# Optimization experiments

Hardware: AMD Instinct MI355X
Metric: run time of the kernel (lower is better)

The kernel has to match this reference:

```python
import jax, jax.numpy as jnp
import numpy as np

N = 50000    # nodes
E = 800000   # edges (avg degree 16)
D_IN = 32
D = 128      # hidden_dim
L = 3        # num_layers
G = 64       # num graphs (sizes.shape[0])
EPS = 1e-5


def gelu(x):
    return jax.nn.gelu(x, approximate=False)  # torch nn.GELU default = exact erf


def layer_norm(x, g, b):
    mu = jnp.mean(x, axis=-1, keepdims=True)
    var = jnp.mean((x - mu) ** 2, axis=-1, keepdims=True)
    return (x - mu) * jax.lax.rsqrt(var + EPS) * g + b


def setup_inputs() -> dict:
    key = jax.random.key(0)
    ks = jax.random.split(key, 16)
    s = 0.02
    inp = {
        "node_features": jax.random.normal(ks[0], (N, D_IN), jnp.float32),
        "edge_index": jax.random.randint(ks[1], (2, E), 0, N),
        "edge_weight": jax.random.uniform(ks[2], (E,), jnp.float32),
        "batch_index": jnp.sort(jax.random.randint(ks[3], (N,), 0, G)),
        "sizes": jnp.ones((G,), jnp.int32),
        # params
        "W_in": jax.random.normal(ks[4], (D_IN, D), jnp.float32) * s,
        "b_in": jnp.zeros((D,), jnp.float32),
        "edge_W1": jax.random.normal(ks[5], (L, 2 * D + 1, D), jnp.float32) * s,
        "edge_b1": jnp.zeros((L, D), jnp.float32),
        "edge_W2": jax.random.normal(ks[6], (L, D, D), jnp.float32) * s,
        "edge_b2": jnp.zeros((L, D), jnp.float32),
        "upd_W1": jax.random.normal(ks[7], (L, 2 * D, D), jnp.float32) * s,
        "upd_b1": jnp.zeros((L, D), jnp.float32),
        "upd_W2": jax.random.normal(ks[8], (L, D, D), jnp.float32) * s,
        "upd_b2": jnp.zeros((L, D), jnp.float32),
        "gamma": jnp.ones((L, D), jnp.float32),
        "beta": jnp.zeros((L, D), jnp.float32),
    }
    return inp


def reference(node_features, edge_index, edge_weight, batch_index, sizes,
              W_in, b_in, edge_W1, edge_b1, edge_W2, edge_b2,
              upd_W1, upd_b1, upd_W2, upd_b2, gamma, beta):
    num_graphs = sizes.shape[0]
    hidden = gelu(node_features @ W_in + b_in)                      # [N, D]
    src, dst = edge_index[0], edge_index[1]
    ew = edge_weight[:, None]                                        # [E, 1]
    for l in range(L):
        edge_inputs = jnp.concatenate([hidden[src], hidden[dst], ew], axis=1)  # [E, 2D+1]
        messages = gelu(edge_inputs @ edge_W1[l] + edge_b1[l]) @ edge_W2[l] + edge_b2[l]
        aggregated = jax.ops.segment_sum(messages, dst, num_segments=N)        # index_add_
        cat = jnp.concatenate([hidden, aggregated], axis=1)                    # [N, 2D]
        updated = gelu(cat @ upd_W1[l] + upd_b1[l]) @ upd_W2[l] + upd_b2[l]
        hidden = layer_norm(hidden + updated, gamma[l], beta[l])
        # dropout p=0.0 -> identity
    counts = jax.ops.segment_sum(jnp.ones((N,), hidden.dtype), batch_index, num_segments=num_graphs)
    pooled = jax.ops.segment_sum(hidden, batch_index, num_segments=num_graphs)
    pooled = pooled / jnp.clip(counts, 1.0)[:, None]                 # graph mean pool
    return hidden, pooled
```

## Files before the change

kernel.cpp:

```cpp
#include <hip/hip_runtime.h>
#include <math.h>

#define NN 50000
#define NE 800000
#define DIN 32
#define D 128
#define NL 3
#define NG 64
#define LN_EPS 1e-5f
#define SCAN_BLOCKS 196

#define PR_T   48
#define PR_W2P (PR_T + 192)
#define PR_B2P (PR_W2P + 2)
#define PR_WIN (PR_B2P + 16)
#define PR_CNT (PR_WIN + 32)
#define PR_TOTAL (PR_CNT + NE / 256)

#define NBLK_IP 782

typedef unsigned short u16;
typedef __bf16 bf16x8 __attribute__((ext_vector_type(8)));
typedef float f32x4 __attribute__((ext_vector_type(4)));

__device__ __forceinline__ float gelu_f(float x) {
    return 0.5f * x * (1.0f + erff(x * 0.70710678118654752f));
}

__device__ __forceinline__ float gelu_fast(float x) {
    float u = x * x;
    float z = x * fmaf(-0.1029432f, u, -2.3022082f);
    float e = __builtin_amdgcn_exp2f(z);
    float s = __builtin_amdgcn_rcpf(1.0f + e);
    return x * s;
}

__device__ __forceinline__ u16 f2bf(float x) {
    unsigned int u = __float_as_uint(x);
    u += 0x7fffu + ((u >> 16) & 1u);
    return (u16)(u >> 16);
}

__global__ __launch_bounds__(256) void scan_emit_kernel(
    const int* __restrict__ hist, int* __restrict__ row_ptr,
    int* __restrict__ cursor)
{
    __shared__ int sc[256];
    __shared__ int red[256];
    const int t = threadIdx.x;
    const int blk = blockIdx.x;
    const int i = blk * 256 + t;
    int orig = (i < NN) ? hist[i] : 0;
    sc[t] = orig;

    int seg = 0;
    if (t < blk) {
        const int4* hp = (const int4*)(hist + t * 256);
#pragma unroll 8
        for (int m = 0; m < 64; ++m) {
            int4 v = hp[m];
            seg += v.x + v.y + v.z + v.w;
        }
    }
    red[t] = seg;
    __syncthreads();
    for (int off = 128; off > 0; off >>= 1) {
        if (t < off) red[t] += red[t + off];
        __syncthreads();
    }

    for (int off = 1; off < 256; off <<= 1) {
        int v = (t >= off) ? sc[t - off] : 0;
        __syncthreads();
        sc[t] += v;
        __syncthreads();
    }
    if (i < NN) {
        int ex = sc[t] - orig + red[0];
        row_ptr[i] = ex;
        cursor[i] = ex;
    }
    if (i == 0) row_ptr[NN] = NE;
}

__global__ __launch_bounds__(256) void prep_kernel(
    const float* __restrict__ eW1, const float* __restrict__ uW1,
    const float* __restrict__ uW2, const float* __restrict__ eW2,
    const float* __restrict__ eb2, const float* __restrict__ Wi,
    const int* __restrict__ batch, const int* __restrict__ dst,
    u16* __restrict__ PWT, u16* __restrict__ NW1T, u16* __restrict__ uW2T,
    float* __restrict__ nb2p, u16* __restrict__ WinT,
    float* __restrict__ counts, int* __restrict__ hist)
{
    __shared__ __attribute__((aligned(16))) float ldsF[64 * 65];
    const int blk = blockIdx.x;
    const int tid = threadIdx.x;
    if (blk < PR_T) {
        const int region = blk / 12;
        const int rl = blk - region * 12;
        const int l = rl >> 2;
        const int tile = rl & 3;
        const int k0 = (tile >> 1) * 64, n0 = (tile & 1) * 64;
        const float* srcp; u16* dstp; int dstRS;
        if (region == 0)      { srcp = eW1 + (size_t)l * 257 * 128;         dstp = PWT  + (size_t)l * 32768;         dstRS = 128; }
        else if (region == 1) { srcp = eW1 + (size_t)l * 257 * 128 + 16384; dstp = PWT  + (size_t)l * 32768 + 16384; dstRS = 128; }
        else if (region == 2) { srcp = uW1 + (size_t)l * 32768;             dstp = NW1T + (size_t)l * 32768;         dstRS = 256; }
        else                  { srcp = uW2 + (size_t)l * 16384;             dstp = uW2T + (size_t)l * 16384;         dstRS = 128; }
        const int rr = tid >> 6, cc = tid & 63;
#pragma unroll
        for (int it = 0; it < 16; ++it) {
            int row = it * 4 + rr;
            ldsF[row * 65 + cc] = srcp[(size_t)(k0 + row) * 128 + n0 + cc];
        }
        __syncthreads();
#pragma unroll
        for (int it = 0; it < 16; ++it) {
            int row = it * 4 + rr;
            dstp[(size_t)(n0 + row) * dstRS + k0 + cc] = f2bf(ldsF[cc * 65 + row]);
        }
    } else if (blk < PR_W2P) {
        int i = (blk - PR_T) * 256 + tid;
        int l = i / 16384;
        int r = i - l * 16384;
        int k = r >> 7, n = r & 127;
        const float* w2row = eW2 + (size_t)l * 16384 + k * 128;
        const float* u1col = uW1 + (size_t)l * 32768 + 128 * 128 + n;
        float s = 0.f;
#pragma unroll 4
        for (int j = 0; j < 128; ++j) s = fmaf(w2row[j], u1col[j * 128], s);
        NW1T[(size_t)l * 32768 + n * 256 + 128 + k] = f2bf(s);
    } else if (blk < PR_B2P) {
        int i = (blk - PR_W2P) * 256 + tid;
        if (i < NL * 128) {
            int l = i >> 7, n = i & 127;
            const float* b2r = eb2 + l * 128;
            const float* u1col = uW1 + (size_t)l * 32768 + 128 * 128 + n;
            float s = 0.f;
#pragma unroll 4
            for (int j = 0; j < 128; ++j) s = fmaf(b2r[j], u1col[j * 128], s);
            nb2p[l * 128 + n] = s;
        }
    } else if (blk < PR_WIN) {
        int i = (blk - PR_B2P) * 256 + tid;
        int n = i >> 5, k = i & 31;
        WinT[n * 32 + k] = f2bf(Wi[k * 128 + n]);
    } else if (blk < PR_CNT) {
        float* s_counts = ldsF;
        if (tid < NG) s_counts[tid] = 0.f;
        __syncthreads();
        int t = (blk - PR_WIN) * 256 + tid;
        const int chunk = (NN + 8191) / 8192;
        int beg = t * chunk, end = beg + chunk;
        if (end > NN) end = NN;
        if (beg < NN) {
            int cur = batch[beg];
            float cnt = 0.f;
            for (int i2 = beg; i2 < end; ++i2) {
                int b2 = batch[i2];
                if (b2 != cur) { atomicAdd(&s_counts[cur], cnt); cur = b2; cnt = 0.f; }
                cnt += 1.f;
            }
            atomicAdd(&s_counts[cur], cnt);
        }
        __syncthreads();
        if (tid < NG) {
            float v = s_counts[tid];
            if (v != 0.f) atomicAdd(&counts[tid], v);
        }
    } else {
        int e = (blk - PR_CNT) * 256 + tid;
        atomicAdd(&hist[dst[e]], 1);
    }
}

__global__ __launch_bounds__(256) void scatter_inproj_kernel(
    const int* __restrict__ src, const int* __restrict__ dstp,
    const float* __restrict__ ew, int* __restrict__ cursor,
    int2* __restrict__ sEdge,
    const float* __restrict__ X, const u16* __restrict__ WinT,
    const float* __restrict__ b, u16* __restrict__ hbf,
    const u16* __restrict__ PWT, u16* __restrict__ P)
{
    __shared__ __attribute__((aligned(16))) u16 lds[64 * 264];
    const int blk = blockIdx.x;
    const int tid = threadIdx.x;

    if (blk >= NBLK_IP) {
        int e = (blk - NBLK_IP) * 256 + tid;
        int d = dstp[e];
        int pos = atomicAdd(&cursor[d], 1);
        int2 v;
        v.x = src[e] << 9;
        v.y = __float_as_int(ew[e]);
        sEdge[pos] = v;
        return;
    }

    u16* sO  = lds;
    u16* sXb = lds + 64 * 136;
    const int n0 = blk * 64;
    const int e = tid >> 2, q = tid & 3;

    {
        const int n = n0 + e;
        unsigned hiw[4], low[4];
        if (n < NN) {
            const float4* xr = (const float4*)(X + (size_t)n * DIN + q * 8);
            float vv[8];
            *(float4*)(vv) = xr[0];
            *(float4*)(vv + 4) = xr[1];
#pragma unroll
            for (int j = 0; j < 4; ++j) {
                u16 h0 = f2bf(vv[2 * j]), h1 = f2bf(vv[2 * j + 1]);
                float f0 = __uint_as_float((unsigned)h0 << 16);
                float f1 = __uint_as_float((unsigned)h1 << 16);
                u16 l0 = f2bf(vv[2 * j] - f0), l1 = f2bf(vv[2 * j + 1] - f1);
                hiw[j] = (unsigned)h0 | ((unsigned)h1 << 16);
                low[j] = (unsigned)l0 | ((unsigned)l1 << 16);
            }
        } else {
#pragma unroll
            for (int j = 0; j < 4; ++j) { hiw[j] = 0u; low[j] = 0u; }
        }
        *(uint4*)(sXb + e * 72 + q * 8)      = *(uint4*)hiw;
        *(uint4*)(sXb + e * 72 + 32 + q * 8) = *(uint4*)low;
    }
    __syncthreads();

    const int lane = tid & 63;
    const int l15 = lane & 15;
    const int quad = lane >> 4;
    const int w = tid >> 6;

    {
        f32x4 acc1[4][2];
#pragma unroll
        for (int mt = 0; mt < 4; ++mt)
#pragma unroll
            for (int nt = 0; nt < 2; ++nt) acc1[mt][nt] = (f32x4){0.f, 0.f, 0.f, 0.f};

        bf16x8 bfw[2];
#pragma unroll
        for (int nt = 0; nt < 2; ++nt)
            bfw[nt] = *(const bf16x8*)(WinT + (size_t)(w * 32 + nt * 16 + l15) * 32 + quad * 8);
#pragma unroll
        for (int mt = 0; mt < 4; ++mt) {
            bf16x8 ah = *(const bf16x8*)(sXb + (mt * 16 + l15) * 72 + quad * 8);
            bf16x8 al = *(const bf16x8*)(sXb + (mt * 16 + l15) * 72 + 32 + quad * 8);
            acc1[mt][0] = __builtin_amdgcn_mfma_f32_16x16x32_bf16(ah, bfw[0], acc1[mt][0], 0, 0, 0);
            acc1[mt][0] = __builtin_amdgcn_mfma_f32_16x16x32_bf16(al, bfw[0], acc1[mt][0], 0, 0, 0);
            acc1[mt][1] = __builtin_amdgcn_mfma_f32_16x16x32_bf16(ah, bfw[1], acc1[mt][1], 0, 0, 0);
            acc1[mt][1] = __builtin_amdgcn_mfma_f32_16x16x32_bf16(al, bfw[1], acc1[mt][1], 0, 0, 0);
        }
#pragma unroll
        for (int mt = 0; mt < 4; ++mt)
#pragma unroll
            for (int nt = 0; nt < 2; ++nt) {
                const int col = w * 32 + nt * 16 + l15;
                const float bb = b[col];
#pragma unroll
                for (int r = 0; r < 4; ++r) {
                    const int row = mt * 16 + quad * 4 + r;
                    sO[row * 136 + col] = f2bf(gelu_f(acc1[mt][nt][r] + bb));
                }
            }
    }
    __syncthreads();

    {
        const int n = n0 + e;
        if (n < NN) {
            uint4* hp = (uint4*)(hbf + (size_t)n * D);
            const u16* so = sO + e * 136;
#pragma unroll
            for (int c = 0; c < 4; ++c) hp[q + c * 4] = *(const uint4*)(so + (q + c * 4) * 8);
        }
    }

    const int nbase4 = w * 64;

    f32x4 accp[4][4];
#pragma unroll
    for (int mt = 0; mt < 4; ++mt)
#pragma unroll
        for (int nt = 0; nt < 4; ++nt) accp[mt][nt] = (f32x4){0.f, 0.f, 0.f, 0.f};

#pragma unroll
    for (int kb = 0; kb < 128; kb += 32) {
        bf16x8 bf[4];
#pragma unroll
        for (int nt = 0; nt < 4; ++nt)
            bf[nt] = *(const bf16x8*)(PWT + (size_t)(nbase4 + nt * 16 + l15) * 128 + quad * 8 + kb);
#pragma unroll
        for (int mt = 0; mt < 4; ++mt) {
            bf16x8 af = *(const bf16x8*)(sO + (mt * 16 + l15) * 136 + quad * 8 + kb);
#pragma unroll
            for (int nt = 0; nt < 4; ++nt)
                accp[mt][nt] = __builtin_amdgcn_mfma_f32_16x16x32_bf16(af, bf[nt], accp[mt][nt], 0, 0, 0);
        }
    }
    __syncthreads();

    u16* sP = lds;
#pragma unroll
    for (int mt = 0; mt < 4; ++mt)
#pragma unroll
        for (int nt = 0; nt < 4; ++nt) {
            const int col = nbase4 + nt * 16 + l15;
#pragma unroll
            for (int r = 0; r < 4; ++r)
                sP[(mt * 16 + quad * 4 + r) * 264 + col] = f2bf(accp[mt][nt][r]);
        }
    __syncthreads();
    {
        const int n = n0 + e;
        if (n < NN) {
            uint4* op = (uint4*)(P + (size_t)n * 256);
            const u16* sp = sP + e * 264;
#pragma unroll
            for (int c = 0; c < 8; ++c) op[q + c * 4] = *(const uint4*)(sp + (q + c * 4) * 8);
        }
    }
}

__global__ __launch_bounds__(256) void edge_csr_kernel(
    const u16* __restrict__ P, const int2* __restrict__ sEdge,
    const int* __restrict__ row_ptr,
    const float* __restrict__ W1last, const float* __restrict__ b1,
    u16* __restrict__ Sbf)
{
    const int n = (blockIdx.x * 256 + threadIdx.x) >> 6;
    if (n >= NN) return;
    const int lane = threadIdx.x & 63;
    const int c2 = lane * 2;
    const unsigned laneoff = (unsigned)(c2 * 2);
    const char* Pb = (const char*)P;

    const float wl0 = W1last[c2], wl1 = W1last[c2 + 1];
    unsigned p2 = *(const unsigned*)(Pb + ((unsigned)n * 512u + 256u + laneoff));
    const float t20 = __uint_as_float(p2 << 16) + b1[c2];
    const float t21 = __uint_as_float(p2 & 0xffff0000u) + b1[c2 + 1];

    float a0 = 0.f, a1 = 0.f;
    const int beg = row_ptr[n];
    const int m = row_ptr[n + 1] - beg;
    const int2* ep = sEdge + beg;
    int i = 0;
    for (; i + 3 < m; i += 4) {
        int2 q0 = ep[i], q1 = ep[i + 1], q2 = ep[i + 2], q3 = ep[i + 3];
        unsigned pa = *(const unsigned*)(Pb + ((unsigned)q0.x + laneoff));
        unsigned pb = *(const unsigned*)(Pb + ((unsigned)q1.x + laneoff));
        unsigned pc = *(const unsigned*)(Pb + ((unsigned)q2.x + laneoff));
        unsigned pd = *(const unsigned*)(Pb + ((unsigned)q3.x + laneoff));
        float w0 = __int_as_float(q0.y), w1 = __int_as_float(q1.y);
        float w2 = __int_as_float(q2.y), w3 = __int_as_float(q3.y);
        a0 += gelu_fast(fmaf(w0, wl0, __uint_as_float(pa << 16) + t20));
        a1 += gelu_fast(fmaf(w0, wl1, __uint_as_float(pa & 0xffff0000u) + t21));
        a0 += gelu_fast(fmaf(w1, wl0, __uint_as_float(pb << 16) + t20));
        a1 += gelu_fast(fmaf(w1, wl1, __uint_as_float(pb & 0xffff0000u) + t21));
        a0 += gelu_fast(fmaf(w2, wl0, __uint_as_float(pc << 16) + t20));
        a1 += gelu_fast(fmaf(w2, wl1, __uint_as_float(pc & 0xffff0000u) + t21));
        a0 += gelu_fast(fmaf(w3, wl0, __uint_as_float(pd << 16) + t20));
        a1 += gelu_fast(fmaf(w3, wl1, __uint_as_float(pd & 0xffff0000u) + t21));
    }
    for (; i < m; ++i) {
        int2 q0 = ep[i];
        unsigned pa = *(const unsigned*)(Pb + ((unsigned)q0.x + laneoff));
        float w0 = __int_as_float(q0.y);
        a0 += gelu_fast(fmaf(w0, wl0, __uint_as_float(pa << 16) + t20));
        a1 += gelu_fast(fmaf(w0, wl1, __uint_as_float(pa & 0xffff0000u) + t21));
    }
    unsigned pk = (unsigned)f2bf(a0) | ((unsigned)f2bf(a1) << 16);
    *(unsigned*)(Sbf + (size_t)n * D + c2) = pk;
}

__global__ __launch_bounds__(256, 3) void node_mfma_kernel(
    const u16* __restrict__ hbf, const u16* __restrict__ Sbf,
    const int* __restrict__ hist,
    const u16* __restrict__ NW1T, const float* __restrict__ ub1,
    const float* __restrict__ nb2p,
    const u16* __restrict__ W2T, const float* __restrict__ b2,
    const float* __restrict__ gamma, const float* __restrict__ beta,
    float* __restrict__ hidden_out, u16* __restrict__ hbf_out,
    const u16* __restrict__ PWTnext, u16* __restrict__ Pout, int write_f32,
    const int* __restrict__ batch, float* __restrict__ pooled)
{
    __shared__ __attribute__((aligned(16))) u16 ldsA[64 * 136 * 2];
    __shared__ float s_cnt[64];
    __shared__ int s_b[64];
    u16* sHa = ldsA;
    u16* sSb = ldsA + 64 * 136;
    float* sR = (float*)ldsA;
    const int tid = threadIdx.x;
    const int n0 = blockIdx.x * 64;

    if (tid < 64) {
        int n = n0 + tid;
        s_b[tid] = (write_f32 && n < NN) ? batch[n] : -1;
        if (n >= NN) n = NN - 1;
        s_cnt[tid] = (float)hist[n];
    }
    {
        const int e = tid >> 2, q = tid & 3;
        int n = n0 + e; if (n >= NN) n = NN - 1;
        const uint4* hs = (const uint4*)(hbf + (size_t)n * D);
        const uint4* ss = (const uint4*)(Sbf + (size_t)n * D);
#pragma unroll
        for (int j = 0; j < 4; ++j) {
            const int c = q * 4 + j;
            *(uint4*)(sHa + e * 136 + c * 8) = hs[c];
            *(uint4*)(sSb + e * 136 + c * 8) = ss[c];
        }
    }
    __syncthreads();

    const int lane = tid & 63;
    const int l15 = lane & 15;
    const int quad = lane >> 4;
    const int nbase = (tid >> 6) * 32;

    f32x4 acc[4][2];
#pragma unroll
    for (int mt = 0; mt < 4; ++mt)
#pragma unroll
        for (int nt = 0; nt < 2; ++nt) acc[mt][nt] = (f32x4){0.f, 0.f, 0.f, 0.f};

    const u16* bp0 = NW1T + (size_t)(nbase + l15) * 256 + quad * 8;
    const u16* bp1 = bp0 + 16 * 256;
#pragma unroll
    for (int kb = 0; kb < 256; kb += 32) {
        bf16x8 bf0 = *(const bf16x8*)(bp0 + kb);
        bf16x8 bf1 = *(const bf16x8*)(bp1 + kb);
        const u16* abase = (kb < 128) ? sHa : sSb;
        const int kk = kb & 127;
#pragma unroll
        for (int mt = 0; mt < 4; ++mt) {
            bf16x8 af = *(const bf16x8*)(abase + (mt * 16 + l15) * 136 + quad * 8 + kk);
            acc[mt][0] = __builtin_amdgcn_mfma_f32_16x16x32_bf16(af, bf0, acc[mt][0], 0, 0, 0);
            acc[mt][1] = __builtin_amdgcn_mfma_f32_16x16x32_bf16(af, bf1, acc[mt][1], 0, 0, 0);
        }
    }
    __syncthreads();

#pragma unroll
    for (int mt = 0; mt < 4; ++mt)
#pragma unroll
        for (int nt = 0; nt < 2; ++nt) {
            const int col = nbase + nt * 16 + l15;
            const float bb = ub1[col];
            const float bp = nb2p[col];
#pragma unroll
            for (int r = 0; r < 4; ++r) {
                const int row = mt * 16 + quad * 4 + r;
                float v = acc[mt][nt][r] + bb + s_cnt[row] * bp;
                sSb[row * 136 + col] = f2bf(gelu_f(v));
            }
        }
    __syncthreads();

    f32x4 acc2[4][2];
#pragma unroll
    for (int mt = 0; mt < 4; ++mt)
#pragma unroll
        for (int nt = 0; nt < 2; ++nt) acc2[mt][nt] = (f32x4){0.f, 0.f, 0.f, 0.f};

    const u16* cp0 = W2T + (size_t)(nbase + l15) * 128 + quad * 8;
    const u16* cp1 = cp0 + 16 * 128;
#pragma unroll
    for (int kb = 0; kb < 128; kb += 32) {
        bf16x8 bf0 = *(const bf16x8*)(cp0 + kb);
        bf16x8 bf1 = *(const bf16x8*)(cp1 + kb);
#pragma unroll
        for (int mt = 0; mt < 4; ++mt) {
            bf16x8 af = *(const bf16x8*)(sSb + (mt * 16 + l15) * 136 + quad * 8 + kb);
            acc2[mt][0] = __builtin_amdgcn_mfma_f32_16x16x32_bf16(af, bf0, acc2[mt][0], 0, 0, 0);
            acc2[mt][1] = __builtin_amdgcn_mfma_f32_16x16x32_bf16(af, bf1, acc2[mt][1], 0, 0, 0);
        }
    }

#pragma unroll
    for (int mt = 0; mt < 4; ++mt)
#pragma unroll
        for (int nt = 0; nt < 2; ++nt) {
            const int col = nbase + nt * 16 + l15;
            const float bb = b2[col];
#pragma unroll
            for (int r = 0; r < 4; ++r) {
                const int row = mt * 16 + quad * 4 + r;
                float h = __uint_as_float((unsigned)sHa[row * 136 + col] << 16);
                acc2[mt][nt][r] += bb + h;
            }
        }
    __syncthreads();

#pragma unroll
    for (int mt = 0; mt < 4; ++mt)
#pragma unroll
        for (int nt = 0; nt < 2; ++nt) {
            const int col = nbase + nt * 16 + l15;
#pragma unroll
            for (int r = 0; r < 4; ++r)
                sR[(mt * 16 + quad * 4 + r) * 132 + col] = acc2[mt][nt][r];
        }
    __syncthreads();

    {
        const int e = tid >> 2, t4 = tid & 3;
        float* rr = sR + e * 132 + t4 * 32;
        float s1 = 0.f, s2 = 0.f;
        float4 v[8];
#pragma unroll
        for (int i = 0; i < 8; ++i) {
            v[i] = *(const float4*)(rr + i * 4);
            s1 += v[i].x + v[i].y + v[i].z + v[i].w;
            s2 += v[i].x * v[i].x + v[i].y * v[i].y + v[i].z * v[i].z + v[i].w * v[i].w;
        }
        s1 += __shfl_xor(s1, 1); s2 += __shfl_xor(s2, 1);
        s1 += __shfl_xor(s1, 2); s2 += __shfl_xor(s2, 2);
        const float mean = s1 * (1.f / 128.f);
        const float var = s2 * (1.f / 128.f) - mean * mean;
        const float rs = rsqrtf(var + LN_EPS);
        u16* hrow = (u16*)(sR + e * 132);
#pragma unroll
        for (int i = 0; i < 8; ++i) {
            const float4 g = *(const float4*)(gamma + t4 * 32 + i * 4);
            const float4 be = *(const float4*)(beta + t4 * 32 + i * 4);
            float4 o;
            o.x = (v[i].x - mean) * rs * g.x + be.x;
            o.y = (v[i].y - mean) * rs * g.y + be.y;
            o.z = (v[i].z - mean) * rs * g.z + be.z;
            o.w = (v[i].w - mean) * rs * g.w + be.w;
            if (write_f32) {
                *(float4*)(rr + i * 4) = o;
            } else {
                uint2 pk;
                pk.x = (unsigned)f2bf(o.x) | ((unsigned)f2bf(o.y) << 16);
                pk.y = (unsigned)f2bf(o.z) | ((unsigned)f2bf(o.w) << 16);
                *(uint2*)(hrow + t4 * 32 + i * 4) = pk;
            }
        }
    }

    if (write_f32) {
        __syncthreads();
        {
            const int e = tid >> 2, q = tid & 3;
            const int n = n0 + e;
            if (n < NN) {
                float4* op = (float4*)(hidden_out + (size_t)n * D);
                const float* sr = sR + e * 132;
#pragma unroll
                for (int c = 0; c < 8; ++c) op[q + c * 4] = *(const float4*)(sr + (q + c * 4) * 4);
            }
        }
        {
            const int col = tid & 127, half = tid >> 7;
            const int base = half * 32;
            int cur = s_b[base];
            float acc_p = 0.f;
            for (int i = 0; i < 32; ++i) {
                int b = s_b[base + i];
                if (b < 0) break;
                if (b != cur) { atomicAdd(&pooled[cur * D + col], acc_p); cur = b; acc_p = 0.f; }
                acc_p += sR[(base + i) * 132 + col];
            }
            if (cur >= 0) atomicAdd(&pooled[cur * D + col], acc_p);
        }
    } else {
        __syncthreads();
        {
            const int e = tid >> 2, q = tid & 3;
            const int n = n0 + e;
            if (n < NN) {
                uint4* hp = (uint4*)(hbf_out + (size_t)n * D);
                const u16* sh = (const u16*)(sR + e * 132);
#pragma unroll
                for (int c = 0; c < 4; ++c) hp[q + c * 4] = *(const uint4*)(sh + (q + c * 4) * 8);
            }
        }
        if (PWTnext) {
            const int nbase4 = (tid >> 6) * 64;
            const u16* sHn = (const u16*)sR;
            f32x4 accp[4][4];
#pragma unroll
            for (int mt = 0; mt < 4; ++mt)
#pragma unroll
                for (int nt = 0; nt < 4; ++nt) accp[mt][nt] = (f32x4){0.f, 0.f, 0.f, 0.f};

#pragma unroll
            for (int kb = 0; kb < 128; kb += 32) {
                bf16x8 bf[4];
#pragma unroll
                for (int nt = 0; nt < 4; ++nt)
                    bf[nt] = *(const bf16x8*)(PWTnext + (size_t)(nbase4 + nt * 16 + l15) * 128 + quad * 8 + kb);
#pragma unroll
                for (int mt = 0; mt < 4; ++mt) {
                    bf16x8 af = *(const bf16x8*)(sHn + (size_t)(mt * 16 + l15) * 264 + quad * 8 + kb);
#pragma unroll
                    for (int nt = 0; nt < 4; ++nt)
                        accp[mt][nt] = __builtin_amdgcn_mfma_f32_16x16x32_bf16(af, bf[nt], accp[mt][nt], 0, 0, 0);
                }
            }
            __syncthreads();
            u16* sP = ldsA;
#pragma unroll
            for (int mt = 0; mt < 4; ++mt)
#pragma unroll
                for (int nt = 0; nt < 4; ++nt) {
                    const int col = nbase4 + nt * 16 + l15;
#pragma unroll
                    for (int r = 0; r < 4; ++r)
                        sP[(mt * 16 + quad * 4 + r) * 264 + col] = f2bf(accp[mt][nt][r]);
                }
            __syncthreads();
            const int e = tid >> 2, q = tid & 3;
            const int n = n0 + e;
            if (n < NN) {
                uint4* op = (uint4*)(Pout + (size_t)n * 256);
                const u16* sp = sP + e * 264;
#pragma unroll
                for (int c = 0; c < 8; ++c) op[q + c * 4] = *(const uint4*)(sp + (q + c * 4) * 8);
            }
        }
    }
}

__global__ __launch_bounds__(256) void pool_div_kernel(
    float* __restrict__ pooled, const float* __restrict__ counts)
{
    int i = blockIdx.x * 256 + threadIdx.x;
    pooled[i] /= fmaxf(counts[i >> 7], 1.0f);
}

extern "C" void kernel_launch(void* const* d_in, const int* in_sizes, int n_in,
                              void* d_out, int out_size, void* d_ws, size_t ws_size,
                              hipStream_t stream) {
    const float* X     = (const float*)d_in[0];
    const int*   eidx  = (const int*)d_in[1];
    const float* ew    = (const float*)d_in[2];
    const int*   batch = (const int*)d_in[3];
    const float* W_in  = (const float*)d_in[5];
    const float* b_in  = (const float*)d_in[6];
    const float* eW1   = (const float*)d_in[7];
    const float* eb1   = (const float*)d_in[8];
    const float* eW2   = (const float*)d_in[9];
    const float* eb2   = (const float*)d_in[10];
    const float* uW1   = (const float*)d_in[11];
    const float* ub1   = (const float*)d_in[12];
    const float* uW2   = (const float*)d_in[13];
    const float* ub2   = (const float*)d_in[14];
    const float* gamma = (const float*)d_in[15];
    const float* beta  = (const float*)d_in[16];

    float* out_hidden = (float*)d_out;
    float* out_pooled = out_hidden + (size_t)NN * D;

    u16*   hbf  = (u16*)d_ws;
    u16*   P    = hbf + (size_t)NN * D;
    u16*   Sbf  = P + (size_t)NN * 256;
    u16*   PWT  = Sbf + (size_t)NN * D;
    u16*   NW1T = PWT + (size_t)NL * 256 * 128;
    u16*   uW2T = NW1T + (size_t)NL * 128 * 256;
    float* nb2p = (float*)(uW2T + (size_t)NL * 128 * 128);
    u16*   WinT = (u16*)(nb2p + (size_t)NL * 128);
    int*   hist    = (int*)(WinT + 128 * 32);
    int*   row_ptr = hist + NN;
    int*   cursor  = row_ptr + NN + 1;
    int*   bsum    = cursor + NN;
    int*   boff    = bsum + SCAN_BLOCKS;
    int2*  sEdge   = (int2*)(boff + SCAN_BLOCKS + 1);
    float* counts  = (float*)(sEdge + NE);

    const int* src = eidx;
    const int* dst = eidx + NE;

    hipMemsetAsync(hist, 0, (size_t)NN * sizeof(int), stream);
    hipMemsetAsync(out_pooled, 0, (size_t)NG * D * sizeof(float), stream);
    hipMemsetAsync(counts, 0, (size_t)NG * sizeof(float), stream);

    prep_kernel<<<PR_TOTAL, 256, 0, stream>>>(
        eW1, uW1, uW2, eW2, eb2, W_in, batch, dst,
        PWT, NW1T, uW2T, nb2p, WinT, counts, hist);

    scan_emit_kernel<<<SCAN_BLOCKS, 256, 0, stream>>>(hist, row_ptr, cursor);

    scatter_inproj_kernel<<<NBLK_IP + NE / 256, 256, 0, stream>>>(
        src, dst, ew, cursor, sEdge, X, WinT, b_in, hbf, PWT, P);

    const int nblk = (NN + 63) / 64;
    for (int l = 0; l < NL; ++l) {
        edge_csr_kernel<<<(NN * 64 + 255) / 256, 256, 0, stream>>>(
            P, sEdge, row_ptr,
            eW1 + (size_t)l * 257 * 128 + 256 * 128,
            eb1 + (size_t)l * D, Sbf);
        const u16* pwt_next = (l < NL - 1) ? (PWT + (size_t)(l + 1) * 256 * 128) : nullptr;
        node_mfma_kernel<<<nblk, 256, 0, stream>>>(
            hbf, Sbf, hist,
            NW1T + (size_t)l * 128 * 256, ub1 + (size_t)l * D, nb2p + (size_t)l * D,
            uW2T + (size_t)l * 128 * 128, ub2 + (size_t)l * D,
            gamma + (size_t)l * D, beta + (size_t)l * D,
            out_hidden, hbf, pwt_next, P, (l == NL - 1) ? 1 : 0,
            batch, out_pooled);
    }

    pool_div_kernel<<<(NG * D) / 256, 256, 0, stream>>>(out_pooled, counts);
}
```

Baseline: 457.1 us.

## Split next-layer projection GEMM into two halves to cut accumulator registers

The projection of the new hidden state onto the next layer's edge weights is computed in two passes of 128 output columns each, with 4x2 accumulator tiles instead of 4x4. The first half is staged into the unused upper part of the LDS row while the hidden tile is still being read, and the second half overwrites the lower part after a barrier. Launch bounds are raised from 3 to 4 blocks per SIMD, so the compiler must fit fewer registers and occupancy can rise. This trades repeated A-operand LDS reads and a less register-blocked MFMA loop for lower register pressure, with possible spilling elsewhere in the kernel.

```diff
diff --git a/kernel.cpp b/kernel.cpp
--- a/kernel.cpp
+++ b/kernel.cpp
@@ -374,7 +374,7 @@
     *(unsigned*)(Sbf + (size_t)n * D + c2) = pk;
 }
 
-__global__ __launch_bounds__(256, 3) void node_mfma_kernel(
+__global__ __launch_bounds__(256, 4) void node_mfma_kernel(
     const u16* __restrict__ hbf, const u16* __restrict__ Sbf,
     const int* __restrict__ hist,
     const u16* __restrict__ NW1T, const float* __restrict__ ub1,
@@ -579,47 +579,73 @@
             }
         }
         if (PWTnext) {
-            const int nbase4 = (tid >> 6) * 64;
             const u16* sHn = (const u16*)sR;
-            f32x4 accp[4][4];
+            u16* sPx = (u16*)sR;
+            const int cbase = (tid >> 6) * 32;
+            f32x4 accp[4][2];
+
 #pragma unroll
             for (int mt = 0; mt < 4; ++mt)
 #pragma unroll
-                for (int nt = 0; nt < 4; ++nt) accp[mt][nt] = (f32x4){0.f, 0.f, 0.f, 0.f};
-
+                for (int nt = 0; nt < 2; ++nt) accp[mt][nt] = (f32x4){0.f, 0.f, 0.f, 0.f};
 #pragma unroll
             for (int kb = 0; kb < 128; kb += 32) {
-                bf16x8 bf[4];
-#pragma unroll
-                for (int nt = 0; nt < 4; ++nt)
-                    bf[nt] = *(const bf16x8*)(PWTnext + (size_t)(nbase4 + nt * 16 + l15) * 128 + quad * 8 + kb);
+                bf16x8 bf0 = *(const bf16x8*)(PWTnext + (size_t)(cbase + l15) * 128 + quad * 8 + kb);
+                bf16x8 bf1 = *(const bf16x8*)(PWTnext + (size_t)(cbase + 16 + l15) * 128 + quad * 8 + kb);
 #pragma unroll
                 for (int mt = 0; mt < 4; ++mt) {
                     bf16x8 af = *(const bf16x8*)(sHn + (size_t)(mt * 16 + l15) * 264 + quad * 8 + kb);
-#pragma unroll
-                    for (int nt = 0; nt < 4; ++nt)
-                        accp[mt][nt] = __builtin_amdgcn_mfma_f32_16x16x32_bf16(af, bf[nt], accp[mt][nt], 0, 0, 0);
+                    accp[mt][0] = __builtin_amdgcn_mfma_f32_16x16x32_bf16(af, bf0, accp[mt][0], 0, 0, 0);
+                    accp[mt][1] = __builtin_amdgcn_mfma_f32_16x16x32_bf16(af, bf1, accp[mt][1], 0, 0, 0);
                 }
             }
+#pragma unroll
+            for (int mt = 0; mt < 4; ++mt)
+#pragma unroll
+                for (int nt = 0; nt < 2; ++nt) {
+                    const int col = cbase + nt * 16 + l15;
+#pragma unroll
+                    for (int r = 0; r < 4; ++r)
+                        sPx[(mt * 16 + quad * 4 + r) * 264 + 128 + col] = f2bf(accp[mt][nt][r]);
+                }
+
+#pragma unroll
+            for (int mt = 0; mt < 4; ++mt)
+#pragma unroll
+                for (int nt = 0; nt < 2; ++nt) accp[mt][nt] = (f32x4){0.f, 0.f, 0.f, 0.f};
+#pragma unroll
+            for (int kb = 0; kb < 128; kb += 32) {
+                bf16x8 bf0 = *(const bf16x8*)(PWTnext + (size_t)(128 + cbase + l15) * 128 + quad * 8 + kb);
+                bf16x8 bf1 = *(const bf16x8*)(PWTnext + (size_t)(128 + cbase + 16 + l15) * 128 + quad * 8 + kb);
+#pragma unroll
+                for (int mt = 0; mt < 4; ++mt) {
+                    bf16x8 af = *(const bf16x8*)(sHn + (size_t)(mt * 16 + l15) * 264 + quad * 8 + kb);
+                    accp[mt][0] = __builtin_amdgcn_mfma_f32_16x16x32_bf16(af, bf0, accp[mt][0], 0, 0, 0);
+                    accp[mt][1] = __builtin_amdgcn_mfma_f32_16x16x32_bf16(af, bf1, accp[mt][1], 0, 0, 0);
+                }
+            }
             __syncthreads();
-            u16* sP = ldsA;
 #pragma unroll
             for (int mt = 0; mt < 4; ++mt)
 #pragma unroll
-                for (int nt = 0; nt < 4; ++nt) {
-                    const int col = nbase4 + nt * 16 + l15;
+                for (int nt = 0; nt < 2; ++nt) {
+                    const int col = cbase + nt * 16 + l15;
 #pragma unroll
                     for (int r = 0; r < 4; ++r)
-                        sP[(mt * 16 + quad * 4 + r) * 264 + col] = f2bf(accp[mt][nt][r]);
+                        sPx[(mt * 16 + quad * 4 + r) * 264 + col] = f2bf(accp[mt][nt][r]);
                 }
             __syncthreads();
-            const int e = tid >> 2, q = tid & 3;
-            const int n = n0 + e;
-            if (n < NN) {
-                uint4* op = (uint4*)(Pout + (size_t)n * 256);
-                const u16* sp = sP + e * 264;
-#pragma unroll
-                for (int c = 0; c < 8; ++c) op[q + c * 4] = *(const uint4*)(sp + (q + c * 4) * 8);
+            const int e2 = tid >> 2, q2 = tid & 3;
+            const int n2 = n0 + e2;
+            if (n2 < NN) {
+                uint4* op = (uint4*)(Pout + (size_t)n2 * 256);
+                const u16* rowp = sPx + e2 * 264;
+#pragma unroll
+                for (int c = 0; c < 4; ++c)
+                    op[q2 + c * 4] = *(const uint4*)(rowp + 128 + (q2 + c * 4) * 8);
+#pragma unroll
+                for (int c = 0; c < 4; ++c)
+                    op[16 + q2 + c * 4] = *(const uint4*)(rowp + (q2 + c * 4) * 8);
             }
         }
     }
```

New measurement: 454.2 us. No clear change (-0.6%).
